# Kernel optimization log

Hardware: AMD Instinct MI355X
Metric: run time of the kernel (lower is better)

Reference implementation:

```python
import jax, jax.numpy as jnp
import numpy as np

B, S, D, E, TOPK, H = 8, 2048, 2048, 8, 2, 16
DH = D // H          # head_dim = 128
FH = D // H          # head_hidden_dim = 128 (hidden == dim, forced by linear3 shapes)
ROUTE_LEN = 2048     # x0 = x[:, :2048]


def setup_inputs() -> dict:
    key = jax.random.key(0)
    ks = jax.random.split(key, 8)
    s = 0.02
    return {
        "x": jax.random.normal(ks[0], (B, S, D), jnp.float32),
        "switch_w": jax.random.normal(ks[1], (E, D * ROUTE_LEN), jnp.float32) * s,
        "switch_b": jnp.zeros((E,), jnp.float32),
        "w1": jax.random.normal(ks[2], (E, FH, DH), jnp.float32) * s,
        "b1": jnp.zeros((E, FH), jnp.float32),
        "w2": jax.random.normal(ks[3], (E, DH, FH), jnp.float32) * s,
        "b2": jnp.zeros((E, DH), jnp.float32),
        "w3": jax.random.normal(ks[4], (D, D), jnp.float32) * s,
        "b3": jnp.zeros((D,), jnp.float32),
    }


def reference(x, switch_w, switch_b, w1, b1, w2, b2, w3, b3):
    b, s, d = x.shape
    # --- router: per batch-sample softmax over experts, top-k selection ---
    x0 = x[:, :ROUTE_LEN].reshape(b, -1)                      # [B, 2048*D]
    logits = x0 @ switch_w.T + switch_b                       # [B, E]
    probs = jax.nn.softmax(logits, axis=-1)
    gate, top_idx = jax.lax.top_k(probs, TOPK)                # [B, K]
    # --- split heads ---
    xh = x.reshape(b, s, H, DH).transpose(0, 2, 1, 3)         # [B, H, S, Dh]
    # --- per-sample gather of selected expert weights (dense grouped GEMM) ---
    w1s, b1s = w1[top_idx], b1[top_idx]                       # [B,K,F,Dh], [B,K,F]
    w2s, b2s = w2[top_idx], b2[top_idx]                       # [B,K,Dh,F], [B,K,Dh]
    h = jnp.einsum('bhsd,bkfd->bkhsf', xh, w1s) + b1s[:, :, None, None, :]
    h = jax.nn.gelu(h, approximate=False)                     # torch nn.GELU is exact
    o = jnp.einsum('bkhsf,bkdf->bkhsd', h, w2s) + b2s[:, :, None, None, :]
    # gate-weighted combine over selected experts (index_add_ sums the k copies)
    o = (o * gate[:, :, None, None, None]).sum(axis=1)        # [B, H, S, Dh]
    o = o.transpose(0, 2, 1, 3).reshape(b, s, d)              # combine heads
    out = x + o                                               # residual
    return out @ w3.T + b3                                    # linear3
```

## Files before the change

### kernel.cpp

```cpp
#include <hip/hip_runtime.h>
#include <math.h>

typedef unsigned short u16;
typedef unsigned int u32;
typedef __attribute__((ext_vector_type(8))) short short8;
typedef __attribute__((ext_vector_type(4))) float f32x4;
typedef __attribute__((ext_vector_type(4))) unsigned short ushort4v;

#define B_ 8
#define S_ 2048
#define D_ 2048
#define H_ 16
#define RLEN 4194304
#define NCHUNK 512

static __device__ __forceinline__ u16 f2bf(float f) {
    union { float f; u32 u; } v; v.f = f;
    u32 r = v.u + 0x7fffu + ((v.u >> 16) & 1u);
    return (u16)(r >> 16);
}
static __device__ __forceinline__ float bf2f(u16 u) {
    union { u32 u; float f; } v; v.u = ((u32)u) << 16;
    return v.f;
}

typedef const __attribute__((address_space(1))) u32* gas1_t;
typedef __attribute__((address_space(3))) u32* las3_t;
static __device__ __forceinline__ void gload_lds16(const void* g, void* l) {
    __builtin_amdgcn_global_load_lds((gas1_t)g, (las3_t)l, 16, 0, 0);
}

template<int XB>
__global__ __launch_bounds__(256) void router_partial(const float* __restrict__ x,
                                                      const float* __restrict__ sw,
                                                      float* __restrict__ part,
                                                      u16* __restrict__ xb) {
    int c = blockIdx.x;
    int t = threadIdx.x;
    const int chunk = RLEN / NCHUNK;
    int base = c * chunk;
    float acc[8][8];
#pragma unroll
    for (int b = 0; b < 8; b++)
#pragma unroll
        for (int e = 0; e < 8; e++) acc[b][e] = 0.f;

    for (int it = 0; it < chunk / (256 * 4); ++it) {
        int i = base + (it * 256 + t) * 4;
        float4 xv[8], sv[8];
#pragma unroll
        for (int b = 0; b < 8; b++) xv[b] = *(const float4*)&x[(size_t)b * RLEN + i];
#pragma unroll
        for (int e = 0; e < 8; e++) sv[e] = *(const float4*)&sw[(size_t)e * RLEN + i];
        if (XB) {
            int row = i >> 7, col = i & 127;
            int scol = (((col >> 3) ^ (row & 7)) << 3) | (col & 7);
#pragma unroll
            for (int b = 0; b < 8; b++) {
                ushort4v u;
                u.x = f2bf(xv[b].x); u.y = f2bf(xv[b].y);
                u.z = f2bf(xv[b].z); u.w = f2bf(xv[b].w);
                *(ushort4v*)&xb[(size_t)b * RLEN + (size_t)row * 128 + scol] = u;
            }
        }
#pragma unroll
        for (int b = 0; b < 8; b++)
#pragma unroll
            for (int e = 0; e < 8; e++)
                acc[b][e] += xv[b].x * sv[e].x + xv[b].y * sv[e].y +
                             xv[b].z * sv[e].z + xv[b].w * sv[e].w;
    }

    __shared__ float red[4][64];
    int lane = t & 63, wv = t >> 6;
#pragma unroll
    for (int q = 0; q < 64; q++) {
        float v = acc[q >> 3][q & 7];
#pragma unroll
        for (int m = 32; m >= 1; m >>= 1) v += __shfl_xor(v, m, 64);
        if (lane == 0) red[wv][q] = v;
    }
    __syncthreads();
    if (t < 64) {
        float s = red[0][t] + red[1][t] + red[2][t] + red[3][t];
        part[(size_t)t * NCHUNK + c] = s;
    }
}

__global__ __launch_bounds__(128) void router_finish(const float* __restrict__ part,
                                                     const float* __restrict__ swb,
                                                     const float* __restrict__ b2,
                                                     float* __restrict__ gate,
                                                     int* __restrict__ idx,
                                                     float* __restrict__ bc) {
    int t = threadIdx.x;
    __shared__ float lg[64];
    __shared__ float sg[16];
    __shared__ int   si[16];
    if (t < 64) {
        float s = 0.f;
        for (int c = 0; c < NCHUNK; c++) s += part[(size_t)t * NCHUNK + c];
        lg[t] = s + swb[t & 7];
    }
    __syncthreads();
    if (t < 8) {
        int b = t;
        float m = -1e30f;
        for (int e = 0; e < 8; e++) m = fmaxf(m, lg[b * 8 + e]);
        float p[8]; float sum = 0.f;
        for (int e = 0; e < 8; e++) { p[e] = expf(lg[b * 8 + e] - m); sum += p[e]; }
        for (int e = 0; e < 8; e++) p[e] /= sum;
        int i1 = 0; float v1 = p[0];
        for (int e = 1; e < 8; e++) if (p[e] > v1) { v1 = p[e]; i1 = e; }
        int i2 = -1; float v2 = -1.f;
        for (int e = 0; e < 8; e++) if (e != i1 && p[e] > v2) { v2 = p[e]; i2 = e; }
        gate[b * 2 + 0] = v1; gate[b * 2 + 1] = v2;
        idx[b * 2 + 0] = i1;  idx[b * 2 + 1] = i2;
        sg[b * 2] = v1; sg[b * 2 + 1] = v2;
        si[b * 2] = i1; si[b * 2 + 1] = i2;
    }
    __syncthreads();
    for (int b = 0; b < 8; b++)
        bc[b * 128 + t] = sg[b * 2] * b2[si[b * 2] * 128 + t] +
                          sg[b * 2 + 1] * b2[si[b * 2 + 1] * 128 + t];
}

__global__ __launch_bounds__(256) void convert_w12(const float* __restrict__ w1,
                                                   const float* __restrict__ w2,
                                                   u16* __restrict__ w1b,
                                                   u16* __restrict__ w2b) {
    int i4 = (blockIdx.x * 256 + threadIdx.x) * 4;
    if (i4 < 131072) {
        int k = i4 & 127, f = (i4 >> 7) & 127;
        float4 v = *(const float4*)&w1[i4];
        int sc = ((((k >> 3) ^ (f & 7)) << 3) | (k & 7));
        ushort4v u;
        u.x = f2bf(v.x); u.y = f2bf(v.y); u.z = f2bf(v.z); u.w = f2bf(v.w);
        *(ushort4v*)&w1b[(i4 & ~127) + sc] = u;
    } else {
        int j = i4 - 131072;
        float4 v = *(const float4*)&w2[j];
        ushort4v u;
        u.x = f2bf(v.x); u.y = f2bf(v.y); u.z = f2bf(v.z); u.w = f2bf(v.w);
        *(ushort4v*)&w2b[j] = u;
    }
}

__global__ __launch_bounds__(256) void convert_w3(const float* __restrict__ w3,
                                                  u16* __restrict__ w3b) {
    size_t i = ((size_t)blockIdx.x * 256 + threadIdx.x) * 4;
    float4 v = *(const float4*)&w3[i];
    u16* d = &w3b[i];
    d[0] = f2bf(v.x); d[1] = f2bf(v.y); d[2] = f2bf(v.z); d[3] = f2bf(v.w);
}

template<int XB>
__global__ __launch_bounds__(512, 2) void mlp_kernel(const void* __restrict__ xsrc_,
                                                     const u16* __restrict__ w1b,
                                                     const u16* __restrict__ w2b,
                                                     const float* __restrict__ b1,
                                                     const float* __restrict__ gate,
                                                     const int* __restrict__ idx,
                                                     const float* __restrict__ bc,
                                                     u16* __restrict__ y) {
    __shared__ __align__(16) u16 w1s[256 * 128];
    __shared__ __align__(16) u16 xs[2][64 * 128];
    __shared__ __align__(16) u16 hb[64 * 256];
    const int t = threadIdx.x, lane = t & 63, w = t >> 6;
    const int wr = w >> 2, wq = w & 3;
    const int b = blockIdx.y, grp = blockIdx.x;
    const size_t xbase = (size_t)b * RLEN;
    const size_t gbase = xbase + (size_t)grp * 65536;
    const int e0 = idx[b * 2], e1 = idx[b * 2 + 1];
    const int slot = wq >> 1;
    const float gw = gate[b * 2 + slot];
    const float* b1p = b1 + (slot ? e1 : e0) * 128;

    float b1v[4];
#pragma unroll
    for (int nt = 0; nt < 4; nt++)
        b1v[nt] = b1p[(wq & 1) * 64 + nt * 16 + (lane & 15)];
    float bcv[2];
#pragma unroll
    for (int n = 0; n < 2; n++)
        bcv[n] = bc[b * 128 + wq * 32 + n * 16 + (lane & 15)];

    short8 w2f[2][8];
#pragma unroll
    for (int n = 0; n < 2; n++) {
        int d = wq * 32 + n * 16 + (lane & 15);
#pragma unroll
        for (int kb = 0; kb < 8; kb++) {
            int e = (kb >= 4) ? e1 : e0;
            int f = (kb & 3) * 32 + (lane >> 4) * 8;
            w2f[n][kb] = *(const short8*)&w2b[((size_t)(e * 128 + d)) * 128 + f];
        }
    }

#pragma unroll
    for (int p = 0; p < 8; p++) {
        int elem = p * 4096 + t * 8;
        int frow = elem >> 7, col = elem & 127;
        int e = (frow >= 128) ? e1 : e0;
        gload_lds16(w1b + ((size_t)(e * 128 + (frow & 127))) * 128 + col,
                    (char*)w1s + elem * 2);
    }
    if (XB) {
        const u16* xbp = (const u16*)xsrc_;
#pragma unroll
        for (int p = 0; p < 2; p++) {
            int elem = p * 4096 + t * 8;
            gload_lds16(xbp + gbase + elem, (char*)&xs[0][0] + elem * 2);
        }
        asm volatile("s_waitcnt vmcnt(0)" ::: "memory");
    } else {
        const float* xf = (const float*)xsrc_;
#pragma unroll
        for (int p = 0; p < 4; p++) {
            int elem = p * 2048 + t * 4;
            int row = elem >> 7, col = elem & 127;
            float4 v = *(const float4*)&xf[gbase + elem];
            ushort4v u;
            u.x = f2bf(v.x); u.y = f2bf(v.y); u.z = f2bf(v.z); u.w = f2bf(v.w);
            *(ushort4v*)((char*)&xs[0][0] + row * 256 +
                         (((col >> 3) ^ (row & 7)) << 4) + (col & 7) * 2) = u;
        }
        asm volatile("s_waitcnt vmcnt(0) lgkmcnt(0)" ::: "memory");
    }
    __builtin_amdgcn_s_barrier();

    for (int tt = 0; tt < 8; ++tt) {
        const u16* xc = &xs[tt & 1][0];
        u16* xn = &xs[(tt + 1) & 1][0];
        float4 pre[4];
        if (tt < 7) {
            if (XB) {
                const u16* xbp = (const u16*)xsrc_;
#pragma unroll
                for (int p = 0; p < 2; p++) {
                    int elem = p * 4096 + t * 8;
                    gload_lds16(xbp + gbase + (tt + 1) * 8192 + elem,
                                (char*)xn + elem * 2);
                }
            } else {
                const float* xf = (const float*)xsrc_;
#pragma unroll
                for (int p = 0; p < 4; p++) {
                    int elem = p * 2048 + t * 4;
                    pre[p] = *(const float4*)&xf[gbase + (tt + 1) * 8192 + elem];
                }
            }
        }

        f32x4 acc1[2][4];
#pragma unroll
        for (int mt = 0; mt < 2; mt++)
#pragma unroll
            for (int nt = 0; nt < 4; nt++) acc1[mt][nt] = (f32x4){0.f, 0.f, 0.f, 0.f};
#pragma unroll
        for (int kb = 0; kb < 4; kb++) {
            int kg = kb * 4 + (lane >> 4);
            int r0 = wr * 32 + (lane & 15);
            int r1 = r0 + 16;
            short8 a0 = *(const short8*)&xc[r0 * 128 + ((kg ^ (r0 & 7)) << 3)];
            short8 a1 = *(const short8*)&xc[r1 * 128 + ((kg ^ (r1 & 7)) << 3)];
#pragma unroll
            for (int nt = 0; nt < 4; nt++) {
                int fr = wq * 64 + nt * 16 + (lane & 15);
                short8 bb = *(const short8*)&w1s[fr * 128 + ((kg ^ (fr & 7)) << 3)];
                acc1[0][nt] = __builtin_amdgcn_mfma_f32_16x16x32_bf16(a0, bb, acc1[0][nt], 0, 0, 0);
                acc1[1][nt] = __builtin_amdgcn_mfma_f32_16x16x32_bf16(a1, bb, acc1[1][nt], 0, 0, 0);
            }
        }

#pragma unroll
        for (int mt = 0; mt < 2; mt++)
#pragma unroll
            for (int nt = 0; nt < 4; nt++) {
                int fcol = wq * 64 + nt * 16 + (lane & 15);
#pragma unroll
                for (int j = 0; j < 4; j++) {
                    int row = wr * 32 + mt * 16 + (lane >> 4) * 4 + j;
                    float v = acc1[mt][nt][j] + b1v[nt];
                    v = 0.5f * v * (1.0f + erff(v * 0.70710678118654752f)) * gw;
                    hb[row * 256 + ((((fcol >> 3) ^ (row & 7)) << 3) | (fcol & 7))] = f2bf(v);
                }
            }
        asm volatile("s_waitcnt lgkmcnt(0)" ::: "memory");
        __builtin_amdgcn_s_barrier();

        if (!XB && tt < 7) {
#pragma unroll
            for (int p = 0; p < 4; p++) {
                int elem = p * 2048 + t * 4;
                int row = elem >> 7, col = elem & 127;
                ushort4v u;
                u.x = f2bf(pre[p].x); u.y = f2bf(pre[p].y);
                u.z = f2bf(pre[p].z); u.w = f2bf(pre[p].w);
                *(ushort4v*)((char*)xn + row * 256 +
                             (((col >> 3) ^ (row & 7)) << 4) + (col & 7) * 2) = u;
            }
        }

        f32x4 acc2[2][2];
#pragma unroll
        for (int mt = 0; mt < 2; mt++)
#pragma unroll
            for (int n = 0; n < 2; n++) acc2[mt][n] = (f32x4){0.f, 0.f, 0.f, 0.f};
#pragma unroll
        for (int kb = 0; kb < 8; kb++) {
            int fg = kb * 4 + (lane >> 4);
            int r0 = wr * 32 + (lane & 15);
            int r1 = r0 + 16;
            short8 a0 = *(const short8*)&hb[r0 * 256 + ((fg ^ (r0 & 7)) << 3)];
            short8 a1 = *(const short8*)&hb[r1 * 256 + ((fg ^ (r1 & 7)) << 3)];
            acc2[0][0] = __builtin_amdgcn_mfma_f32_16x16x32_bf16(a0, w2f[0][kb], acc2[0][0], 0, 0, 0);
            acc2[0][1] = __builtin_amdgcn_mfma_f32_16x16x32_bf16(a0, w2f[1][kb], acc2[0][1], 0, 0, 0);
            acc2[1][0] = __builtin_amdgcn_mfma_f32_16x16x32_bf16(a1, w2f[0][kb], acc2[1][0], 0, 0, 0);
            acc2[1][1] = __builtin_amdgcn_mfma_f32_16x16x32_bf16(a1, w2f[1][kb], acc2[1][1], 0, 0, 0);
        }

        u16* yb = y + xbase + (size_t)grp * 65536 + tt * 8192;
#pragma unroll
        for (int mt = 0; mt < 2; mt++)
#pragma unroll
            for (int n = 0; n < 2; n++) {
                int d = wq * 32 + n * 16 + (lane & 15);
#pragma unroll
                for (int j = 0; j < 4; j++) {
                    int row = wr * 32 + mt * 16 + (lane >> 4) * 4 + j;
                    float xr = bf2f(xc[row * 128 + ((((d >> 3) ^ (row & 7)) << 3) | (d & 7))]);
                    yb[row * 128 + d] = f2bf(acc2[mt][n][j] + bcv[n] + xr);
                }
            }
        asm volatile("s_waitcnt lgkmcnt(0)" ::: "memory");
        if (XB && tt < 7) asm volatile("s_waitcnt vmcnt(16)" ::: "memory");
        __builtin_amdgcn_s_barrier();
    }
}

#define BARX() do { asm volatile("" ::: "memory"); __builtin_amdgcn_s_barrier(); \
                    asm volatile("" ::: "memory"); } while (0)

#define WLG(NSTR) do { asm volatile("s_waitcnt lgkmcnt(" NSTR ")" ::: "memory"); \
                       __builtin_amdgcn_sched_barrier(0); } while (0)

#define DSA(mh, c) do { \
    const char* _ba = smem + (c) * 65536 + abase; \
    _Pragma("unroll") for (int mf = 0; mf < 4; mf++) \
    _Pragma("unroll") for (int kk = 0; kk < 2; kk++) \
        areg[mf][kk] = *(const short8*)(_ba + ((mh) * 4 + mf) * 2048 + kof[kk]); \
} while (0)

#define DSB(nh, c) do { \
    const char* _bb = smem + (c) * 65536 + bbase; \
    _Pragma("unroll") for (int nf = 0; nf < 2; nf++) \
    _Pragma("unroll") for (int kk = 0; kk < 2; kk++) \
        breg[(nh) * 2 + nf][kk] = *(const short8*)(_bb + ((nh) * 2 + nf) * 2048 + kof[kk]); \
} while (0)

#define MMAQ(mh, nh) do { \
    __builtin_amdgcn_s_setprio(1); \
    _Pragma("unroll") for (int mf = 0; mf < 4; mf++) \
    _Pragma("unroll") for (int nf = 0; nf < 2; nf++) \
    _Pragma("unroll") for (int kk = 0; kk < 2; kk++) \
        acc[(mh) * 4 + mf][(nh) * 2 + nf] = __builtin_amdgcn_mfma_f32_16x16x32_bf16( \
            areg[mf][kk], breg[(nh) * 2 + nf][kk], acc[(mh) * 4 + mf][(nh) * 2 + nf], 0, 0, 0); \
    __builtin_amdgcn_s_setprio(0); \
} while (0)

#define STG(op, c, h, kt) do { \
    const u16* _gs = (op) ? wbp : yap; \
    int _tr0 = (op) ? nrow0 : mrow0; \
    _Pragma("unroll") for (int p = 0; p < 2; p++) { \
        int _idx = p * 512 + t; \
        int _row = _idx >> 3; \
        int _gcol = (((_idx & 7) ^ (_row & 7)) << 3); \
        gload_lds16(_gs + (size_t)(_tr0 + (h) * 128 + _row) * 2048 + (kt) * 64 + _gcol, \
                    smem + (c) * 65536 + (op) * 32768 + (h) * 16384 + _idx * 16); \
    } \
} while (0)

__global__ __launch_bounds__(512, 2) void final_gemm256(const u16* __restrict__ yap,
                                                        const u16* __restrict__ wbp,
                                                        const float* __restrict__ b3,
                                                        float* __restrict__ out) {
    extern __shared__ char smem[];
    const int t = threadIdx.x;
    const int lane = t & 63, w = t >> 6;
    const int wm = w >> 2, wn = w & 3;
    const int l15 = lane & 15, l4 = lane >> 4, sx = lane & 7;

    int bid = blockIdx.x;
    int swz = (bid & 7) * 64 + (bid >> 3);
    int nblk = swz >> 6, mblk = swz & 63;
    const int mrow0 = mblk * 256;
    const int nrow0 = nblk * 256;

    const int abase = wm * 16384 + l15 * 128;
    const int bbase = 32768 + (wn >> 1) * 16384 + ((wn & 1) * 64 + l15) * 128;
    int kof[2];
#pragma unroll
    for (int kk = 0; kk < 2; kk++) kof[kk] = ((kk * 4 + l4) ^ sx) << 4;

    f32x4 acc[8][4];
#pragma unroll
    for (int m = 0; m < 8; m++)
#pragma unroll
        for (int n = 0; n < 4; n++) acc[m][n] = (f32x4){0.f, 0.f, 0.f, 0.f};
    short8 areg[4][2];
    short8 breg[4][2];

    STG(0, 0, 0, 0); STG(0, 0, 1, 0); STG(1, 0, 0, 0); STG(1, 0, 1, 0);
    STG(0, 1, 0, 1); STG(0, 1, 1, 1); STG(1, 1, 0, 1); STG(1, 1, 1, 1);
    asm volatile("s_waitcnt vmcnt(8)" ::: "memory");
    BARX();
    DSA(0, 0); DSB(0, 0); DSB(1, 0);

    for (int it2 = 0; it2 < 16; ++it2) {
#pragma unroll
        for (int c = 0; c < 2; ++c) {
            const int tt = 2 * it2 + c;
            WLG("4");  MMAQ(0, 0);
            WLG("0");  MMAQ(0, 1);
            DSA(1, c);
            WLG("0");  MMAQ(1, 0);
            asm volatile("s_waitcnt vmcnt(0)" ::: "memory");
            BARX();
            if (tt < 30) { STG(0, c, 0, tt + 2); STG(0, c, 1, tt + 2);
                           STG(1, c, 0, tt + 2); STG(1, c, 1, tt + 2); }
            MMAQ(1, 1);
            if (tt < 31) { DSA(0, c ^ 1); DSB(0, c ^ 1); DSB(1, c ^ 1); }
        }
    }

#pragma unroll
    for (int m = 0; m < 8; m++)
#pragma unroll
        for (int n = 0; n < 4; n++) {
            int col = nrow0 + wn * 64 + n * 16 + l15;
            float bias = b3[col];
            int row = mrow0 + wm * 128 + m * 16 + l4 * 4;
#pragma unroll
            for (int j = 0; j < 4; j++)
                out[(size_t)(row + j) * 2048 + col] = acc[m][n][j] + bias;
        }
}

extern "C" void kernel_launch(void* const* d_in, const int* in_sizes, int n_in,
                              void* d_out, int out_size, void* d_ws, size_t ws_size,
                              hipStream_t stream) {
    const float* x   = (const float*)d_in[0];
    const float* sw  = (const float*)d_in[1];
    const float* swb = (const float*)d_in[2];
    const float* w1  = (const float*)d_in[3];
    const float* b1  = (const float*)d_in[4];
    const float* w2  = (const float*)d_in[5];
    const float* b2  = (const float*)d_in[6];
    const float* w3  = (const float*)d_in[7];
    const float* b3  = (const float*)d_in[8];
    float* out = (float*)d_out;

    char* ws = (char*)d_ws;
    float* part = (float*)(ws + 0);
    float* gate = (float*)(ws + 131072);
    int*   idx  = (int*)(ws + 131136);
    float* bc   = (float*)(ws + 131200);
    u16*   w1b  = (u16*)(ws + 262144);
    u16*   w2b  = (u16*)(ws + 524288);
    u16*   w3b  = (u16*)(ws + 786432);
    u16*   y    = (u16*)(ws + 9175040);
    u16*   xb   = (u16*)(ws + 76283904);
    const size_t need_xb = 143392768;
    const bool xbmode = ws_size >= need_xb;

    hipFuncSetAttribute((const void*)final_gemm256,
                        hipFuncAttributeMaxDynamicSharedMemorySize, 131072);

    if (xbmode)
        hipLaunchKernelGGL((router_partial<1>), dim3(NCHUNK), dim3(256), 0, stream, x, sw, part, xb);
    else
        hipLaunchKernelGGL((router_partial<0>), dim3(NCHUNK), dim3(256), 0, stream, x, sw, part, xb);
    hipLaunchKernelGGL(router_finish, dim3(1), dim3(128), 0, stream, part, swb, b2, gate, idx, bc);
    hipLaunchKernelGGL(convert_w12, dim3(256), dim3(256), 0, stream, w1, w2, w1b, w2b);
    hipLaunchKernelGGL(convert_w3, dim3(D_ * D_ / 1024), dim3(256), 0, stream, w3, w3b);
    if (xbmode)
        hipLaunchKernelGGL((mlp_kernel<1>), dim3(64, 8), dim3(512), 0, stream,
                           (const void*)xb, w1b, w2b, b1, gate, idx, bc, y);
    else
        hipLaunchKernelGGL((mlp_kernel<0>), dim3(64, 8), dim3(512), 0, stream,
                           (const void*)x, w1b, w2b, b1, gate, idx, bc, y);
    hipLaunchKernelGGL(final_gemm256, dim3(512), dim3(512), 131072, stream,
                       y, w3b, b3, out);
}
```

Before: 334.0 us.

## Software-pipeline MLP kernel, use tanh GELU, reschedule linear3 GEMM stages

The MLP kernel is restructured into 32-row sub-tiles with a double-buffered h buffer, so the first GEMM and GELU of the next sub-tile are interleaved with the second GEMM of the current one. The min-blocks launch bound is dropped. Exact erf GELU is replaced by a tanh-style approximation built from exp and a hardware reciprocal. The linear3 GEMM main loop is rewritten with finer-grained load/barrier interleaving per quarter tile. This risks a small accuracy loss from the GELU approximation and more barriers in the GEMM loop.

After: 334.8 us. No clear change (+0.3%).

```diff
diff --git a/kernel.cpp b/kernel.cpp
--- a/kernel.cpp
+++ b/kernel.cpp
@@ -22,6 +22,12 @@
 static __device__ __forceinline__ float bf2f(u16 u) {
     union { u32 u; float f; } v; v.u = ((u32)u) << 16;
     return v.f;
+}
+static __device__ __forceinline__ float gelu_fast(float v) {
+    float z = 1.5957691216057308f * v * (1.0f + 0.044715f * v * v);
+    float e = __expf(z);
+    float r = __builtin_amdgcn_rcpf(e + 1.0f);
+    return v * (1.0f - r);
 }
 
 typedef const __attribute__((address_space(1))) u32* gas1_t;
@@ -155,19 +161,20 @@
 }
 
 template<int XB>
-__global__ __launch_bounds__(512, 2) void mlp_kernel(const void* __restrict__ xsrc_,
-                                                     const u16* __restrict__ w1b,
-                                                     const u16* __restrict__ w2b,
-                                                     const float* __restrict__ b1,
-                                                     const float* __restrict__ gate,
-                                                     const int* __restrict__ idx,
-                                                     const float* __restrict__ bc,
-                                                     u16* __restrict__ y) {
+__global__ __launch_bounds__(512) void mlp_kernel(const void* __restrict__ xsrc_,
+                                                  const u16* __restrict__ w1b,
+                                                  const u16* __restrict__ w2b,
+                                                  const float* __restrict__ b1,
+                                                  const float* __restrict__ gate,
+                                                  const int* __restrict__ idx,
+                                                  const float* __restrict__ bc,
+                                                  u16* __restrict__ y) {
     __shared__ __align__(16) u16 w1s[256 * 128];
     __shared__ __align__(16) u16 xs[2][64 * 128];
-    __shared__ __align__(16) u16 hb[64 * 256];
+    __shared__ __align__(16) u16 hb[2][32 * 256];
     const int t = threadIdx.x, lane = t & 63, w = t >> 6;
     const int wr = w >> 2, wq = w & 3;
+    const int l15 = lane & 15, l4 = lane >> 4;
     const int b = blockIdx.y, grp = blockIdx.x;
     const size_t xbase = (size_t)b * RLEN;
     const size_t gbase = xbase + (size_t)grp * 65536;
@@ -178,21 +185,19 @@
 
     float b1v[4];
 #pragma unroll
-    for (int nt = 0; nt < 4; nt++)
-        b1v[nt] = b1p[(wq & 1) * 64 + nt * 16 + (lane & 15)];
+    for (int nt = 0; nt < 4; nt++) b1v[nt] = b1p[(wq & 1) * 64 + nt * 16 + l15];
     float bcv[2];
 #pragma unroll
-    for (int n = 0; n < 2; n++)
-        bcv[n] = bc[b * 128 + wq * 32 + n * 16 + (lane & 15)];
+    for (int n = 0; n < 2; n++) bcv[n] = bc[b * 128 + wq * 32 + n * 16 + l15];
 
     short8 w2f[2][8];
 #pragma unroll
     for (int n = 0; n < 2; n++) {
-        int d = wq * 32 + n * 16 + (lane & 15);
+        int d = wq * 32 + n * 16 + l15;
 #pragma unroll
         for (int kb = 0; kb < 8; kb++) {
             int e = (kb >= 4) ? e1 : e0;
-            int f = (kb & 3) * 32 + (lane >> 4) * 8;
+            int f = (kb & 3) * 32 + l4 * 8;
             w2f[n][kb] = *(const short8*)&w2b[((size_t)(e * 128 + d)) * 128 + f];
         }
     }
@@ -208,142 +213,141 @@
     if (XB) {
         const u16* xbp = (const u16*)xsrc_;
 #pragma unroll
-        for (int p = 0; p < 2; p++) {
-            int elem = p * 4096 + t * 8;
-            gload_lds16(xbp + gbase + elem, (char*)&xs[0][0] + elem * 2);
-        }
+        for (int T = 0; T < 2; T++)
+            gload_lds16(xbp + gbase + T * 8192 + t * 8, (char*)&xs[T][0] + t * 16);
+#pragma unroll
+        for (int T = 0; T < 2; T++)
+            gload_lds16(xbp + gbase + T * 8192 + 4096 + t * 8,
+                        (char*)&xs[T][0] + 8192 + t * 16);
         asm volatile("s_waitcnt vmcnt(0)" ::: "memory");
     } else {
         const float* xf = (const float*)xsrc_;
 #pragma unroll
-        for (int p = 0; p < 4; p++) {
-            int elem = p * 2048 + t * 4;
-            int row = elem >> 7, col = elem & 127;
-            float4 v = *(const float4*)&xf[gbase + elem];
-            ushort4v u;
-            u.x = f2bf(v.x); u.y = f2bf(v.y); u.z = f2bf(v.z); u.w = f2bf(v.w);
-            *(ushort4v*)((char*)&xs[0][0] + row * 256 +
-                         (((col >> 3) ^ (row & 7)) << 4) + (col & 7) * 2) = u;
-        }
-        asm volatile("s_waitcnt vmcnt(0) lgkmcnt(0)" ::: "memory");
-    }
-    __builtin_amdgcn_s_barrier();
-
-    for (int tt = 0; tt < 8; ++tt) {
-        const u16* xc = &xs[tt & 1][0];
-        u16* xn = &xs[(tt + 1) & 1][0];
-        float4 pre[4];
-        if (tt < 7) {
-            if (XB) {
-                const u16* xbp = (const u16*)xsrc_;
-#pragma unroll
-                for (int p = 0; p < 2; p++) {
-                    int elem = p * 4096 + t * 8;
-                    gload_lds16(xbp + gbase + (tt + 1) * 8192 + elem,
-                                (char*)xn + elem * 2);
-                }
-            } else {
-                const float* xf = (const float*)xsrc_;
-#pragma unroll
-                for (int p = 0; p < 4; p++) {
-                    int elem = p * 2048 + t * 4;
-                    pre[p] = *(const float4*)&xf[gbase + (tt + 1) * 8192 + elem];
-                }
-            }
-        }
-
-        f32x4 acc1[2][4];
-#pragma unroll
-        for (int mt = 0; mt < 2; mt++)
-#pragma unroll
-            for (int nt = 0; nt < 4; nt++) acc1[mt][nt] = (f32x4){0.f, 0.f, 0.f, 0.f};
-#pragma unroll
-        for (int kb = 0; kb < 4; kb++) {
-            int kg = kb * 4 + (lane >> 4);
-            int r0 = wr * 32 + (lane & 15);
-            int r1 = r0 + 16;
-            short8 a0 = *(const short8*)&xc[r0 * 128 + ((kg ^ (r0 & 7)) << 3)];
-            short8 a1 = *(const short8*)&xc[r1 * 128 + ((kg ^ (r1 & 7)) << 3)];
-#pragma unroll
-            for (int nt = 0; nt < 4; nt++) {
-                int fr = wq * 64 + nt * 16 + (lane & 15);
-                short8 bb = *(const short8*)&w1s[fr * 128 + ((kg ^ (fr & 7)) << 3)];
-                acc1[0][nt] = __builtin_amdgcn_mfma_f32_16x16x32_bf16(a0, bb, acc1[0][nt], 0, 0, 0);
-                acc1[1][nt] = __builtin_amdgcn_mfma_f32_16x16x32_bf16(a1, bb, acc1[1][nt], 0, 0, 0);
-            }
-        }
-
-#pragma unroll
-        for (int mt = 0; mt < 2; mt++)
-#pragma unroll
-            for (int nt = 0; nt < 4; nt++) {
-                int fcol = wq * 64 + nt * 16 + (lane & 15);
-#pragma unroll
-                for (int j = 0; j < 4; j++) {
-                    int row = wr * 32 + mt * 16 + (lane >> 4) * 4 + j;
-                    float v = acc1[mt][nt][j] + b1v[nt];
-                    v = 0.5f * v * (1.0f + erff(v * 0.70710678118654752f)) * gw;
-                    hb[row * 256 + ((((fcol >> 3) ^ (row & 7)) << 3) | (fcol & 7))] = f2bf(v);
-                }
-            }
-        asm volatile("s_waitcnt lgkmcnt(0)" ::: "memory");
-        __builtin_amdgcn_s_barrier();
-
-        if (!XB && tt < 7) {
+        for (int T = 0; T < 2; T++)
 #pragma unroll
             for (int p = 0; p < 4; p++) {
                 int elem = p * 2048 + t * 4;
                 int row = elem >> 7, col = elem & 127;
+                float4 v = *(const float4*)&xf[gbase + T * 8192 + elem];
                 ushort4v u;
-                u.x = f2bf(pre[p].x); u.y = f2bf(pre[p].y);
-                u.z = f2bf(pre[p].z); u.w = f2bf(pre[p].w);
-                *(ushort4v*)((char*)xn + row * 256 +
+                u.x = f2bf(v.x); u.y = f2bf(v.y); u.z = f2bf(v.z); u.w = f2bf(v.w);
+                *(ushort4v*)((char*)&xs[T][0] + row * 256 +
                              (((col >> 3) ^ (row & 7)) << 4) + (col & 7) * 2) = u;
             }
-        }
-
-        f32x4 acc2[2][2];
-#pragma unroll
-        for (int mt = 0; mt < 2; mt++)
-#pragma unroll
-            for (int n = 0; n < 2; n++) acc2[mt][n] = (f32x4){0.f, 0.f, 0.f, 0.f};
+        asm volatile("s_waitcnt vmcnt(0) lgkmcnt(0)" ::: "memory");
+    }
+    __builtin_amdgcn_s_barrier();
+
+    auto G1 = [&](int st, f32x4* a1) {
+        const u16* xc = &xs[(st >> 1) & 1][0];
+        int rbase = (st & 1) * 32 + wr * 16 + l15;
+#pragma unroll
+        for (int nt = 0; nt < 4; nt++) a1[nt] = (f32x4){0.f, 0.f, 0.f, 0.f};
+#pragma unroll
+        for (int kb = 0; kb < 4; kb++) {
+            int kg = kb * 4 + l4;
+            short8 a = *(const short8*)&xc[rbase * 128 + ((kg ^ (rbase & 7)) << 3)];
+#pragma unroll
+            for (int nt = 0; nt < 4; nt++) {
+                int fr = wq * 64 + nt * 16 + l15;
+                short8 bb = *(const short8*)&w1s[fr * 128 + ((kg ^ (fr & 7)) << 3)];
+                a1[nt] = __builtin_amdgcn_mfma_f32_16x16x32_bf16(a, bb, a1[nt], 0, 0, 0);
+            }
+        }
+    };
+    auto GELU_ST = [&](int st, f32x4* a1) {
+        u16* hd = &hb[st & 1][0];
+#pragma unroll
+        for (int nt = 0; nt < 4; nt++) {
+            int fcol = wq * 64 + nt * 16 + l15;
+#pragma unroll
+            for (int j = 0; j < 4; j++) {
+                int row = wr * 16 + l4 * 4 + j;
+                float v = a1[nt][j] + b1v[nt];
+                v = gelu_fast(v) * gw;
+                hd[row * 256 + ((((fcol >> 3) ^ (row & 7)) << 3) | (fcol & 7))] = f2bf(v);
+            }
+        }
+    };
+    auto G2 = [&](int st, f32x4* a2) {
+        const u16* hs = &hb[st & 1][0];
+        int arow = wr * 16 + l15;
+        a2[0] = (f32x4){0.f, 0.f, 0.f, 0.f};
+        a2[1] = (f32x4){0.f, 0.f, 0.f, 0.f};
 #pragma unroll
         for (int kb = 0; kb < 8; kb++) {
-            int fg = kb * 4 + (lane >> 4);
-            int r0 = wr * 32 + (lane & 15);
-            int r1 = r0 + 16;
-            short8 a0 = *(const short8*)&hb[r0 * 256 + ((fg ^ (r0 & 7)) << 3)];
-            short8 a1 = *(const short8*)&hb[r1 * 256 + ((fg ^ (r1 & 7)) << 3)];
-            acc2[0][0] = __builtin_amdgcn_mfma_f32_16x16x32_bf16(a0, w2f[0][kb], acc2[0][0], 0, 0, 0);
-            acc2[0][1] = __builtin_amdgcn_mfma_f32_16x16x32_bf16(a0, w2f[1][kb], acc2[0][1], 0, 0, 0);
-            acc2[1][0] = __builtin_amdgcn_mfma_f32_16x16x32_bf16(a1, w2f[0][kb], acc2[1][0], 0, 0, 0);
-            acc2[1][1] = __builtin_amdgcn_mfma_f32_16x16x32_bf16(a1, w2f[1][kb], acc2[1][1], 0, 0, 0);
-        }
-
-        u16* yb = y + xbase + (size_t)grp * 65536 + tt * 8192;
-#pragma unroll
-        for (int mt = 0; mt < 2; mt++)
-#pragma unroll
-            for (int n = 0; n < 2; n++) {
-                int d = wq * 32 + n * 16 + (lane & 15);
-#pragma unroll
-                for (int j = 0; j < 4; j++) {
-                    int row = wr * 32 + mt * 16 + (lane >> 4) * 4 + j;
-                    float xr = bf2f(xc[row * 128 + ((((d >> 3) ^ (row & 7)) << 3) | (d & 7))]);
-                    yb[row * 128 + d] = f2bf(acc2[mt][n][j] + bcv[n] + xr);
+            int fg = kb * 4 + l4;
+            short8 a = *(const short8*)&hs[arow * 256 + ((fg ^ (arow & 7)) << 3)];
+            a2[0] = __builtin_amdgcn_mfma_f32_16x16x32_bf16(a, w2f[0][kb], a2[0], 0, 0, 0);
+            a2[1] = __builtin_amdgcn_mfma_f32_16x16x32_bf16(a, w2f[1][kb], a2[1], 0, 0, 0);
+        }
+    };
+    auto YST = [&](int st, f32x4* a2) {
+        const u16* xc = &xs[(st >> 1) & 1][0];
+        u16* yb = y + xbase + (size_t)grp * 65536 + st * 4096;
+#pragma unroll
+        for (int n = 0; n < 2; n++) {
+            int d = wq * 32 + n * 16 + l15;
+#pragma unroll
+            for (int j = 0; j < 4; j++) {
+                int row = wr * 16 + l4 * 4 + j;
+                int xrow = (st & 1) * 32 + row;
+                float xr = bf2f(xc[xrow * 128 + ((((d >> 3) ^ (xrow & 7)) << 3) | (d & 7))]);
+                yb[row * 128 + d] = f2bf(a2[n][j] + bcv[n] + xr);
+            }
+        }
+    };
+
+    {
+        f32x4 a1[4];
+        G1(0, a1);
+        GELU_ST(0, a1);
+    }
+    asm volatile("s_waitcnt lgkmcnt(0)" ::: "memory");
+    __builtin_amdgcn_s_barrier();
+
+    for (int st = 0; st < 16; ++st) {
+        const bool stg = ((st & 1) == 0) && st >= 2 && st <= 12;
+        if (stg) {
+            int T = st / 2 + 1;
+            if (XB) {
+                const u16* xbp = (const u16*)xsrc_;
+                gload_lds16(xbp + gbase + T * 8192 + t * 8, (char*)&xs[T & 1][0] + t * 16);
+                gload_lds16(xbp + gbase + T * 8192 + 4096 + t * 8,
+                            (char*)&xs[T & 1][0] + 8192 + t * 16);
+            } else {
+                const float* xf = (const float*)xsrc_;
+#pragma unroll
+                for (int p = 0; p < 4; p++) {
+                    int elem = p * 2048 + t * 4;
+                    int row = elem >> 7, col = elem & 127;
+                    float4 v = *(const float4*)&xf[gbase + T * 8192 + elem];
+                    ushort4v u;
+                    u.x = f2bf(v.x); u.y = f2bf(v.y); u.z = f2bf(v.z); u.w = f2bf(v.w);
+                    *(ushort4v*)((char*)&xs[T & 1][0] + row * 256 +
+                                 (((col >> 3) ^ (row & 7)) << 4) + (col & 7) * 2) = u;
                 }
             }
+        }
+        f32x4 a1n[4];
+        if (st < 15) G1(st + 1, a1n);
+        f32x4 a2[2];
+        G2(st, a2);
+        if (st < 15) GELU_ST(st + 1, a1n);
+        YST(st, a2);
         asm volatile("s_waitcnt lgkmcnt(0)" ::: "memory");
-        if (XB && tt < 7) asm volatile("s_waitcnt vmcnt(16)" ::: "memory");
+        if (stg && XB) asm volatile("s_waitcnt vmcnt(8)" ::: "memory");
+        if (stg && !XB) asm volatile("s_waitcnt vmcnt(0)" ::: "memory");
         __builtin_amdgcn_s_barrier();
     }
 }
 
 #define BARX() do { asm volatile("" ::: "memory"); __builtin_amdgcn_s_barrier(); \
                     asm volatile("" ::: "memory"); } while (0)
-
-#define WLG(NSTR) do { asm volatile("s_waitcnt lgkmcnt(" NSTR ")" ::: "memory"); \
-                       __builtin_amdgcn_sched_barrier(0); } while (0)
+#define WLGC(NSTR) do { asm volatile("s_waitcnt lgkmcnt(" NSTR ")" ::: "memory"); \
+                        __builtin_amdgcn_sched_barrier(0); } while (0)
+#define WVMC(NSTR) do { asm volatile("s_waitcnt vmcnt(" NSTR ")" ::: "memory"); \
+                        __builtin_amdgcn_sched_barrier(0); } while (0)
 
 #define DSA(mh, c) do { \
     const char* _ba = smem + (c) * 65536 + abase; \
@@ -412,26 +416,55 @@
     short8 breg[4][2];
 
     STG(0, 0, 0, 0); STG(0, 0, 1, 0); STG(1, 0, 0, 0); STG(1, 0, 1, 0);
-    STG(0, 1, 0, 1); STG(0, 1, 1, 1); STG(1, 1, 0, 1); STG(1, 1, 1, 1);
-    asm volatile("s_waitcnt vmcnt(8)" ::: "memory");
+    STG(0, 1, 0, 1); STG(1, 1, 0, 1); STG(1, 1, 1, 1); STG(0, 1, 1, 1);
+    WVMC("8");
     BARX();
-    DSA(0, 0); DSB(0, 0); DSB(1, 0);
-
-    for (int it2 = 0; it2 < 16; ++it2) {
-#pragma unroll
-        for (int c = 0; c < 2; ++c) {
-            const int tt = 2 * it2 + c;
-            WLG("4");  MMAQ(0, 0);
-            WLG("0");  MMAQ(0, 1);
-            DSA(1, c);
-            WLG("0");  MMAQ(1, 0);
-            asm volatile("s_waitcnt vmcnt(0)" ::: "memory");
-            BARX();
-            if (tt < 30) { STG(0, c, 0, tt + 2); STG(0, c, 1, tt + 2);
-                           STG(1, c, 0, tt + 2); STG(1, c, 1, tt + 2); }
-            MMAQ(1, 1);
-            if (tt < 31) { DSA(0, c ^ 1); DSB(0, c ^ 1); DSB(1, c ^ 1); }
-        }
+
+    for (int tt = 0; tt < 30; ++tt) {
+        const int c = tt & 1;
+        DSA(0, c); DSB(0, c);
+        if (tt >= 1) STG(1, c ^ 1, 1, tt + 1);
+        WLGC("8");
+        BARX(); WLGC("0"); MMAQ(0, 0);
+        WVMC("8"); BARX();
+        DSB(1, c);
+        if (tt >= 1) STG(0, c ^ 1, 1, tt + 1);
+        BARX(); WLGC("0"); MMAQ(0, 1);
+        WVMC("8"); BARX();
+        DSA(1, c);
+        STG(0, c, 0, tt + 2);
+        BARX(); WLGC("0"); MMAQ(1, 0);
+        WVMC("8"); BARX();
+        STG(1, c, 0, tt + 2);
+        BARX(); MMAQ(1, 1);
+        WVMC("8"); BARX();
+    }
+    {
+        const int c = 0;
+        DSA(0, c); DSB(0, c); STG(1, c ^ 1, 1, 31);
+        WLGC("8"); BARX(); WLGC("0"); MMAQ(0, 0);
+        WVMC("8"); BARX();
+        DSB(1, c); STG(0, c ^ 1, 1, 31);
+        BARX(); WLGC("0"); MMAQ(0, 1);
+        WVMC("8"); BARX();
+        DSA(1, c);
+        BARX(); WLGC("0"); MMAQ(1, 0);
+        WVMC("4"); BARX();
+        BARX(); MMAQ(1, 1);
+        WVMC("4"); BARX();
+    }
+    {
+        const int c = 1;
+        DSA(0, c); DSB(0, c);
+        WLGC("8"); BARX(); WLGC("0"); MMAQ(0, 0);
+        WVMC("2"); BARX();
+        DSB(1, c);
+        BARX(); WLGC("0"); MMAQ(0, 1);
+        WVMC("0"); BARX();
+        DSA(1, c);
+        BARX(); WLGC("0"); MMAQ(1, 0);
+        BARX();
+        MMAQ(1, 1);
     }
 
 #pragma unroll
```
